# Kernel optimization log

Measured on AMD Instinct MI355X. Metric: run time of the kernel, lower is better.

The kernel has to match this reference:

```python
import jax, jax.numpy as jnp
import numpy as np

N, IN_DIM, H1, H2, HEADS = 3072, 256, 128, 64, 4
NEG_INF = -9.0e15  # matches torch zero_vec = -9e15

def _xavier(key, shape):
    fan_in, fan_out = shape[-2], shape[-1]
    lim = np.sqrt(6.0 / (fan_in + fan_out)).astype(np.float32)
    return jax.random.uniform(key, shape, jnp.float32, -lim, lim)

def setup_inputs() -> dict:
    key = jax.random.key(0)
    ks = jax.random.split(key, 14)
    x = jax.random.normal(ks[0], (N, IN_DIM), jnp.float32)
    adj = jax.random.randint(ks[1], (N, N), 0, 2, jnp.int32)
    # layer 1 params (per-head stacked)
    W1 = _xavier(ks[2], (HEADS, IN_DIM, H1))
    a1s = _xavier(ks[3], (HEADS, H1)) * 1.414   # a[:F] of the (2F,1) xavier vector
    a1d = _xavier(ks[4], (HEADS, H1)) * 1.414   # a[F:]
    lin1 = _xavier(ks[5], (HEADS * H1, H1))
    res1 = _xavier(ks[6], (IN_DIM, H1))
    # layer 2 params
    W2 = _xavier(ks[7], (HEADS, H1, H2))
    a2s = _xavier(ks[8], (HEADS, H2)) * 1.414
    a2d = _xavier(ks[9], (HEADS, H2)) * 1.414
    lin2 = _xavier(ks[10], (HEADS * H2, H2))
    res2 = _xavier(ks[11], (H1, H2))
    return {"x": x, "adj": adj, "W1": W1, "a1s": a1s, "a1d": a1d,
            "lin1": lin1, "res1": res1, "W2": W2, "a2s": a2s, "a2d": a2d,
            "lin2": lin2, "res2": res2}

def _gat_residual_layer(h, mask, W, a_s, a_d, lin, res):
    # h: [N, F_in], W: [H, F_in, F_out], mask: [N, N] bool
    Wh = jnp.einsum('nf,hfo->hno', h, W)                 # [H, N, F_out]
    src = jnp.einsum('hno,ho->hn', Wh, a_s)              # Wh @ a[:F]
    dst = jnp.einsum('hno,ho->hn', Wh, a_d)              # Wh @ a[F:]
    e = src[:, :, None] + dst[:, None, :]                # [H, N, N]
    e = jnp.where(e > 0, e, 0.2 * e)                     # leaky_relu(0.2)
    e = jnp.where(mask[None], e, NEG_INF)                # adj mask
    attn = jax.nn.softmax(e, axis=-1)                    # dropout p=0.1 -> identity (eval)
    hp = jax.nn.elu(jnp.einsum('hij,hjo->hio', attn, Wh))  # per-head output, elu
    n = h.shape[0]
    hp = jnp.transpose(hp, (1, 0, 2)).reshape(n, -1)     # concat heads (head-major)
    hp = jax.nn.elu(hp @ lin)                            # multi-head mix + elu
    out = jax.nn.relu(hp + h @ res)                      # residual + relu
    return jax.nn.relu(out)                              # encoder-loop relu; dropout(0.4) identity

def reference(x, adj, W1, a1s, a1d, lin1, res1, W2, a2s, a2d, lin2, res2):
    mask = adj > 0
    h = _gat_residual_layer(x, mask, W1, a1s, a1d, lin1, res1)
    h = _gat_residual_layer(h, mask, W2, a2s, a2d, lin2, res2)
    return h  # embedding [N, H2]
```

## Files before the change

kernel.cpp:

```cpp
#include <hip/hip_runtime.h>
#include <hip/hip_bf16.h>
#include <stdint.h>

using bf16 = __hip_bfloat16;
typedef short short8 __attribute__((ext_vector_type(8)));
typedef short short4v __attribute__((ext_vector_type(4)));
typedef float f32x4 __attribute__((ext_vector_type(4)));

constexpr int N = 3072;
constexpr int D0 = 256;
constexpr int F1 = 128;
constexpr int F2 = 64;
constexpr int HEADS = 4;
constexpr int NW = N / 32;
constexpr float CSHIFT = 20.0f;

#define DI __device__ __forceinline__
DI short f2bs(float v) { bf16 b = __float2bfloat16(v); return *(short*)&b; }

__global__ __launch_bounds__(256) void k_pack_adj(const int* __restrict__ adj,
                                                  uint32_t* __restrict__ bits) {
  int idx = blockIdx.x * 256 + threadIdx.x;
  unsigned long long m = __ballot(adj[idx] > 0);
  if ((threadIdx.x & 63) == 0) {
    bits[idx >> 5]       = (uint32_t)m;
    bits[(idx >> 5) + 1] = (uint32_t)(m >> 32);
  }
}

__global__ __launch_bounds__(256) void k_cvt(const float* __restrict__ x,
                                             const float* __restrict__ W1,
                                             const float* __restrict__ lin1,
                                             const float* __restrict__ res1,
                                             const float* __restrict__ W2,
                                             const float* __restrict__ lin2,
                                             const float* __restrict__ res2,
                                             bf16* __restrict__ xb,
                                             bf16* __restrict__ W1T,
                                             bf16* __restrict__ lin1T,
                                             bf16* __restrict__ res1T,
                                             bf16* __restrict__ W2T,
                                             bf16* __restrict__ lin2T,
                                             bf16* __restrict__ res2T) {
  int t = blockIdx.y;
  int i = blockIdx.x * 256 + threadIdx.x;
  switch (t) {
    case 0:
      if (i < N * D0) xb[i] = __float2bfloat16(x[i]);
      break;
    case 1:
      if (i < HEADS * F1 * D0) { int k = i & 255; int ho = i >> 8; int h = ho >> 7, o = ho & 127;
        W1T[i] = __float2bfloat16(W1[((size_t)h * D0 + k) * F1 + o]); }
      break;
    case 2:
      if (i < F1 * HEADS * F1) { int k = i & 511; int o = i >> 9;
        lin1T[i] = __float2bfloat16(lin1[k * F1 + o]); }
      break;
    case 3:
      if (i < F1 * D0) { int k = i & 255; int o = i >> 8;
        res1T[i] = __float2bfloat16(res1[k * F1 + o]); }
      break;
    case 4:
      if (i < HEADS * F2 * F1) { int k = i & 127; int ho = i >> 7; int h = ho >> 6, o = ho & 63;
        W2T[i] = __float2bfloat16(W2[((size_t)h * F1 + k) * F2 + o]); }
      break;
    case 5:
      if (i < F2 * HEADS * F2) { int k = i & 255; int o = i >> 8;
        lin2T[i] = __float2bfloat16(lin2[k * F2 + o]); }
      break;
    case 6:
      if (i < F2 * F1) { int k = i & 127; int o = i >> 7;
        res2T[i] = __float2bfloat16(res2[k * F2 + o]); }
      break;
  }
}

template <int K, int NOUT, int F>
__global__ __launch_bounds__(256) void k_whead_mfma(const bf16* __restrict__ A,
                                                    const bf16* __restrict__ BT,
                                                    bf16* __restrict__ BP,
                                                    const float* __restrict__ as_,
                                                    const float* __restrict__ ad_,
                                                    float* __restrict__ src,
                                                    float* __restrict__ dst) {
  int row0 = blockIdx.x * 16;
  int wid = threadIdx.x >> 6, lane = threadIdx.x & 63;
  int l15 = lane & 15, q = lane >> 4;
  int col = blockIdx.y * 64 + wid * 16 + l15;

  const bf16* aP = A + (size_t)(row0 + l15) * K + q * 8;
  const bf16* bP = BT + (size_t)col * K + q * 8;
  f32x4 acc;
#pragma unroll
  for (int r = 0; r < 4; r++) acc[r] = 0.f;
#pragma unroll
  for (int ks = 0; ks < K / 32; ks++) {
    short8 a = *(const short8*)(aP + ks * 32);
    short8 b = *(const short8*)(bP + ks * 32);
    acc = __builtin_amdgcn_mfma_f32_16x16x32_bf16(a, b, acc, 0, 0, 0);
  }

  int h  = col / F;
  int cl = col % F;
  int ct = cl >> 4;
  int jt = row0 >> 5;
  int qp = ((row0 >> 4) & 1) * 2 + (q >> 1);
  int eo = (q & 1) * 4;
  short4v w;
#pragma unroll
  for (int r = 0; r < 4; r++) w[r] = f2bs(acc[r]);
  size_t off = ((((size_t)h * (F / 16) + ct) * (N / 32) + jt) * 4 + qp) * 128 + l15 * 8 + eo;
  *(short4v*)(BP + off) = w;

  float asv = as_[col], adv = ad_[col];
#pragma unroll
  for (int r = 0; r < 4; r++) {
    float sp = acc[r] * asv, dp = acc[r] * adv;
#pragma unroll
    for (int m = 1; m < 16; m <<= 1) {
      sp += __shfl_xor(sp, m);
      dp += __shfl_xor(dp, m);
    }
    if (l15 == 0) {
      atomicAdd(&src[h * N + row0 + q * 4 + r], sp);
      atomicAdd(&dst[h * N + row0 + q * 4 + r], dp);
    }
  }
}

template <int F>
__global__ __launch_bounds__(256, 2) void k_attn_fused(const bf16* __restrict__ BP,
                                                       const float* __restrict__ src,
                                                       const float* __restrict__ dst,
                                                       const uint32_t* __restrict__ bits,
                                                       float* __restrict__ hp_part,
                                                       float* __restrict__ rs_part) {
  constexpr int CT = F / 16;
  constexpr int CTN = CT / 4;
  constexpr int KSTEPS = 12;
  int h    = blockIdx.y;
  int kb   = blockIdx.z;
  int row0 = blockIdx.x * 32;
  int tid = threadIdx.x, wid = tid >> 6, lane = tid & 63;
  int l15 = lane & 15, q = lane >> 4;
  int jbase = kb * (N / 2) + wid * 384;

  float src0 = src[h * N + row0 + l15];
  float src1 = src[h * N + row0 + 16 + l15];
  const float* dh = dst + h * N;
  const uint32_t* b0 = bits + (size_t)(row0 + l15) * NW;
  const uint32_t* b1 = bits + (size_t)(row0 + 16 + l15) * NW;
  const bf16* bph = BP + (size_t)h * CT * (N / 32) * 512;

  f32x4 acc0[CT], acc1[CT];
#pragma unroll
  for (int ct = 0; ct < CT; ct++)
#pragma unroll
    for (int r = 0; r < 4; r++) { acc0[ct][r] = 0.f; acc1[ct][r] = 0.f; }
  float rs0 = 0.f, rs1 = 0.f;

  for (int ks = 0; ks < KSTEPS; ks++) {
    int j0 = jbase + ks * 32;
    int jt = j0 >> 5;
    f32x4 dlo = *(const f32x4*)(dh + j0 + q * 8);
    f32x4 dhi = *(const f32x4*)(dh + j0 + q * 8 + 4);
    uint32_t m0 = (b0[jt] >> (q * 8)) & 0xffu;
    uint32_t m1 = (b1[jt] >> (q * 8)) & 0xffu;
    float pv0[8], pv1[8];
#pragma unroll
    for (int e = 0; e < 8; e++) {
      float d = e < 4 ? dlo[e] : dhi[e - 4];
      float t0 = src0 + d; t0 = fmaxf(t0, 0.2f * t0);
      float p0 = ((m0 >> e) & 1u) ? __expf(t0 - CSHIFT) : 0.f;
      rs0 += p0; pv0[e] = p0;
      float t1 = src1 + d; t1 = fmaxf(t1, 0.2f * t1);
      float p1 = ((m1 >> e) & 1u) ? __expf(t1 - CSHIFT) : 0.f;
      rs1 += p1; pv1[e] = p1;
    }
    short8 a0, a1;
#pragma unroll
    for (int e = 0; e < 8; e++) { a0[e] = f2bs(pv0[e]); a1[e] = f2bs(pv1[e]); }
#pragma unroll
    for (int ct = 0; ct < CT; ct++) {
      short8 b = *(const short8*)(bph + (((size_t)ct * (N / 32) + jt) * 64 + lane) * 8);
      acc0[ct] = __builtin_amdgcn_mfma_f32_16x16x32_bf16(a0, b, acc0[ct], 0, 0, 0);
      acc1[ct] = __builtin_amdgcn_mfma_f32_16x16x32_bf16(a1, b, acc1[ct], 0, 0, 0);
    }
  }

  rs0 += __shfl_xor(rs0, 16); rs0 += __shfl_xor(rs0, 32);
  rs1 += __shfl_xor(rs1, 16); rs1 += __shfl_xor(rs1, 32);
  if (q == 0) atomicAdd(&rs_part[((size_t)kb * HEADS + h) * N + row0 + l15], rs0);
  if (q == 1) atomicAdd(&rs_part[((size_t)kb * HEADS + h) * N + row0 + 16 + l15], rs1);

  __shared__ float red[4][64][CT * 4 + 1];
#pragma unroll
  for (int t = 0; t < 2; t++) {
    __syncthreads();
#pragma unroll
    for (int ct = 0; ct < CT; ct++)
#pragma unroll
      for (int r = 0; r < 4; r++)
        red[wid][lane][ct * 4 + r] = t ? acc1[ct][r] : acc0[ct][r];
    __syncthreads();
#pragma unroll
    for (int cc = 0; cc < CTN; cc++) {
      int ct = wid * CTN + cc;
#pragma unroll
      for (int r = 0; r < 4; r++) {
        float v = red[0][lane][ct * 4 + r] + red[1][lane][ct * 4 + r] +
                  red[2][lane][ct * 4 + r] + red[3][lane][ct * 4 + r];
        int row = row0 + t * 16 + q * 4 + r;
        hp_part[((size_t)kb * N + row) * (HEADS * F) + h * F + ct * 16 + l15] = v;
      }
    }
  }
}

template <int K1, int K2, int NOUT, int F, bool F32OUT>
__global__ __launch_bounds__(256) void k_mix_mfma(const float* __restrict__ hpp,
                                                  const float* __restrict__ rs,
                                                  const bf16* __restrict__ B1T,
                                                  const bf16* __restrict__ A2,
                                                  const bf16* __restrict__ B2T,
                                                  void* __restrict__ outv) {
  int row0 = blockIdx.x * 16;
  int wid = threadIdx.x >> 6, lane = threadIdx.x & 63;
  int l15 = lane & 15, q = lane >> 4;
  int col = blockIdx.y * 64 + wid * 16 + l15;
  int row = row0 + l15;

  f32x4 acc1, acc2;
#pragma unroll
  for (int r = 0; r < 4; r++) { acc1[r] = 0.f; acc2[r] = 0.f; }

  const float* p0 = hpp + (size_t)row * K1;
  const float* p1 = hpp + ((size_t)N + row) * K1;
  const bf16* b1P = B1T + (size_t)col * K1 + q * 8;
#pragma unroll
  for (int ks = 0; ks < K1 / 32; ks++) {
    int h = (ks * 32) / F;
    float s = rs[h * N + row] + rs[(HEADS + h) * N + row];
    float inv = 1.f / s;
    int c0k = ks * 32 + q * 8;
    f32x4 x0 = *(const f32x4*)(p0 + c0k);
    f32x4 x1 = *(const f32x4*)(p0 + c0k + 4);
    f32x4 y0 = *(const f32x4*)(p1 + c0k);
    f32x4 y1 = *(const f32x4*)(p1 + c0k + 4);
    short8 a;
#pragma unroll
    for (int e = 0; e < 4; e++) {
      float v = (x0[e] + y0[e]) * inv;
      v = v > 0.f ? v : __expf(v) - 1.f;
      a[e] = f2bs(v);
    }
#pragma unroll
    for (int e = 0; e < 4; e++) {
      float v = (x1[e] + y1[e]) * inv;
      v = v > 0.f ? v : __expf(v) - 1.f;
      a[4 + e] = f2bs(v);
    }
    short8 b = *(const short8*)(b1P + ks * 32);
    acc1 = __builtin_amdgcn_mfma_f32_16x16x32_bf16(a, b, acc1, 0, 0, 0);
  }

  const bf16* a2P = A2 + (size_t)row * K2 + q * 8;
  const bf16* b2P = B2T + (size_t)col * K2 + q * 8;
#pragma unroll
  for (int ks = 0; ks < K2 / 32; ks++) {
    short8 a = *(const short8*)(a2P + ks * 32);
    short8 b = *(const short8*)(b2P + ks * 32);
    acc2 = __builtin_amdgcn_mfma_f32_16x16x32_bf16(a, b, acc2, 0, 0, 0);
  }

#pragma unroll
  for (int r = 0; r < 4; r++) {
    float v = acc1[r];
    v = v > 0.f ? v : __expf(v) - 1.f;
    v += acc2[r];
    v = v > 0.f ? v : 0.f;
    int rw = row0 + q * 4 + r;
    if (F32OUT) ((float*)outv)[(size_t)rw * NOUT + col] = v;
    else        ((bf16*)outv)[(size_t)rw * NOUT + col] = __float2bfloat16(v);
  }
}

extern "C" void kernel_launch(void* const* d_in, const int* in_sizes, int n_in,
                              void* d_out, int out_size, void* d_ws, size_t ws_size,
                              hipStream_t stream) {
  const float* x    = (const float*)d_in[0];
  const int*   adj  = (const int*)d_in[1];
  const float* W1   = (const float*)d_in[2];
  const float* a1s  = (const float*)d_in[3];
  const float* a1d  = (const float*)d_in[4];
  const float* lin1 = (const float*)d_in[5];
  const float* res1 = (const float*)d_in[6];
  const float* W2   = (const float*)d_in[7];
  const float* a2s  = (const float*)d_in[8];
  const float* a2d  = (const float*)d_in[9];
  const float* lin2 = (const float*)d_in[10];
  const float* res2 = (const float*)d_in[11];
  float* out = (float*)d_out;

  char* p = (char*)d_ws;
  auto alloc = [&](size_t bytes) { void* r = (void*)p; p += (bytes + 255) & ~(size_t)255; return r; };
  uint32_t* bits = (uint32_t*)alloc((size_t)N * NW * 4);
  bf16* xb    = (bf16*)alloc((size_t)N * D0 * 2);
  bf16* W1T   = (bf16*)alloc((size_t)HEADS * F1 * D0 * 2);
  bf16* lin1T = (bf16*)alloc((size_t)F1 * HEADS * F1 * 2);
  bf16* res1T = (bf16*)alloc((size_t)F1 * D0 * 2);
  bf16* W2T   = (bf16*)alloc((size_t)HEADS * F2 * F1 * 2);
  bf16* lin2T = (bf16*)alloc((size_t)F2 * HEADS * F2 * 2);
  bf16* res2T = (bf16*)alloc((size_t)F2 * F1 * 2);
  bf16* BP1   = (bf16*)alloc((size_t)HEADS * F1 * N * 2);
  bf16* BP2   = (bf16*)alloc((size_t)HEADS * F2 * N * 2);
  float* src1 = (float*)alloc((size_t)HEADS * N * 4);
  float* dst1 = (float*)alloc((size_t)HEADS * N * 4);
  float* src2 = (float*)alloc((size_t)HEADS * N * 4);
  float* dst2 = (float*)alloc((size_t)HEADS * N * 4);
  float* rs1  = (float*)alloc((size_t)2 * HEADS * N * 4);
  float* rs2  = (float*)alloc((size_t)2 * HEADS * N * 4);
  float* hpp1 = (float*)alloc((size_t)2 * N * HEADS * F1 * 4);
  float* hpp2 = (float*)alloc((size_t)2 * N * HEADS * F2 * 4);
  bf16* h1b   = (bf16*)alloc((size_t)N * F1 * 2);

  hipMemsetAsync(src1, 0, (size_t)HEADS * N * 4 * 8, stream);

  k_pack_adj<<<dim3(N * N / 256), dim3(256), 0, stream>>>(adj, bits);
  k_cvt<<<dim3(N * D0 / 256, 7), dim3(256), 0, stream>>>(x, W1, lin1, res1, W2, lin2, res2,
                                                         xb, W1T, lin1T, res1T, W2T, lin2T, res2T);

  k_whead_mfma<D0, HEADS * F1, F1>
      <<<dim3(N / 16, HEADS * F1 / 64), dim3(256), 0, stream>>>(xb, W1T, BP1, a1s, a1d, src1, dst1);
  k_attn_fused<F1><<<dim3(N / 32, HEADS, 2), dim3(256), 0, stream>>>(BP1, src1, dst1, bits, hpp1, rs1);
  k_mix_mfma<HEADS * F1, D0, F1, F1, false>
      <<<dim3(N / 16, F1 / 64), dim3(256), 0, stream>>>(hpp1, rs1, lin1T, xb, res1T, h1b);

  k_whead_mfma<F1, HEADS * F2, F2>
      <<<dim3(N / 16, HEADS * F2 / 64), dim3(256), 0, stream>>>(h1b, W2T, BP2, a2s, a2d, src2, dst2);
  k_attn_fused<F2><<<dim3(N / 32, HEADS, 2), dim3(256), 0, stream>>>(BP2, src2, dst2, bits, hpp2, rs2);
  k_mix_mfma<HEADS * F2, F1, F2, F2, true>
      <<<dim3(N / 16, 1), dim3(256), 0, stream>>>(hpp2, rs2, lin2T, h1b, res2T, out);
}
```

Measured before the change: 215.2 us.

## Shrink attention row tile to 16 and use single-wave blocks for GEMMs

```diff
diff --git a/kernel.cpp b/kernel.cpp
--- a/kernel.cpp
+++ b/kernel.cpp
@@ -76,17 +76,17 @@
 }
 
 template <int K, int NOUT, int F>
-__global__ __launch_bounds__(256) void k_whead_mfma(const bf16* __restrict__ A,
-                                                    const bf16* __restrict__ BT,
-                                                    bf16* __restrict__ BP,
-                                                    const float* __restrict__ as_,
-                                                    const float* __restrict__ ad_,
-                                                    float* __restrict__ src,
-                                                    float* __restrict__ dst) {
+__global__ __launch_bounds__(64) void k_whead_mfma(const bf16* __restrict__ A,
+                                                   const bf16* __restrict__ BT,
+                                                   bf16* __restrict__ BP,
+                                                   const float* __restrict__ as_,
+                                                   const float* __restrict__ ad_,
+                                                   float* __restrict__ src,
+                                                   float* __restrict__ dst) {
   int row0 = blockIdx.x * 16;
-  int wid = threadIdx.x >> 6, lane = threadIdx.x & 63;
+  int lane = threadIdx.x;
   int l15 = lane & 15, q = lane >> 4;
-  int col = blockIdx.y * 64 + wid * 16 + l15;
+  int col = blockIdx.y * 16 + l15;
 
   const bf16* aP = A + (size_t)(row0 + l15) * K + q * 8;
   const bf16* bP = BT + (size_t)col * K + q * 8;
@@ -129,35 +129,33 @@
 }
 
 template <int F>
-__global__ __launch_bounds__(256, 2) void k_attn_fused(const bf16* __restrict__ BP,
-                                                       const float* __restrict__ src,
-                                                       const float* __restrict__ dst,
-                                                       const uint32_t* __restrict__ bits,
-                                                       float* __restrict__ hp_part,
-                                                       float* __restrict__ rs_part) {
+__global__ __launch_bounds__(256) void k_attn_fused(const bf16* __restrict__ BP,
+                                                    const float* __restrict__ src,
+                                                    const float* __restrict__ dst,
+                                                    const uint32_t* __restrict__ bits,
+                                                    float* __restrict__ hp_part,
+                                                    float* __restrict__ rs_part) {
   constexpr int CT = F / 16;
   constexpr int CTN = CT / 4;
   constexpr int KSTEPS = 12;
   int h    = blockIdx.y;
   int kb   = blockIdx.z;
-  int row0 = blockIdx.x * 32;
+  int row0 = blockIdx.x * 16;
   int tid = threadIdx.x, wid = tid >> 6, lane = tid & 63;
   int l15 = lane & 15, q = lane >> 4;
   int jbase = kb * (N / 2) + wid * 384;
 
   float src0 = src[h * N + row0 + l15];
-  float src1 = src[h * N + row0 + 16 + l15];
   const float* dh = dst + h * N;
   const uint32_t* b0 = bits + (size_t)(row0 + l15) * NW;
-  const uint32_t* b1 = bits + (size_t)(row0 + 16 + l15) * NW;
   const bf16* bph = BP + (size_t)h * CT * (N / 32) * 512;
 
-  f32x4 acc0[CT], acc1[CT];
+  f32x4 acc0[CT];
 #pragma unroll
   for (int ct = 0; ct < CT; ct++)
 #pragma unroll
-    for (int r = 0; r < 4; r++) { acc0[ct][r] = 0.f; acc1[ct][r] = 0.f; }
-  float rs0 = 0.f, rs1 = 0.f;
+    for (int r = 0; r < 4; r++) acc0[ct][r] = 0.f;
+  float rs0 = 0.f;
 
   for (int ks = 0; ks < KSTEPS; ks++) {
     int j0 = jbase + ks * 32;
@@ -165,69 +163,57 @@
     f32x4 dlo = *(const f32x4*)(dh + j0 + q * 8);
     f32x4 dhi = *(const f32x4*)(dh + j0 + q * 8 + 4);
     uint32_t m0 = (b0[jt] >> (q * 8)) & 0xffu;
-    uint32_t m1 = (b1[jt] >> (q * 8)) & 0xffu;
-    float pv0[8], pv1[8];
+    float pv0[8];
 #pragma unroll
     for (int e = 0; e < 8; e++) {
       float d = e < 4 ? dlo[e] : dhi[e - 4];
       float t0 = src0 + d; t0 = fmaxf(t0, 0.2f * t0);
       float p0 = ((m0 >> e) & 1u) ? __expf(t0 - CSHIFT) : 0.f;
       rs0 += p0; pv0[e] = p0;
-      float t1 = src1 + d; t1 = fmaxf(t1, 0.2f * t1);
-      float p1 = ((m1 >> e) & 1u) ? __expf(t1 - CSHIFT) : 0.f;
-      rs1 += p1; pv1[e] = p1;
-    }
-    short8 a0, a1;
-#pragma unroll
-    for (int e = 0; e < 8; e++) { a0[e] = f2bs(pv0[e]); a1[e] = f2bs(pv1[e]); }
+    }
+    short8 a0;
+#pragma unroll
+    for (int e = 0; e < 8; e++) a0[e] = f2bs(pv0[e]);
 #pragma unroll
     for (int ct = 0; ct < CT; ct++) {
       short8 b = *(const short8*)(bph + (((size_t)ct * (N / 32) + jt) * 64 + lane) * 8);
       acc0[ct] = __builtin_amdgcn_mfma_f32_16x16x32_bf16(a0, b, acc0[ct], 0, 0, 0);
-      acc1[ct] = __builtin_amdgcn_mfma_f32_16x16x32_bf16(a1, b, acc1[ct], 0, 0, 0);
     }
   }
 
   rs0 += __shfl_xor(rs0, 16); rs0 += __shfl_xor(rs0, 32);
-  rs1 += __shfl_xor(rs1, 16); rs1 += __shfl_xor(rs1, 32);
   if (q == 0) atomicAdd(&rs_part[((size_t)kb * HEADS + h) * N + row0 + l15], rs0);
-  if (q == 1) atomicAdd(&rs_part[((size_t)kb * HEADS + h) * N + row0 + 16 + l15], rs1);
 
   __shared__ float red[4][64][CT * 4 + 1];
 #pragma unroll
-  for (int t = 0; t < 2; t++) {
-    __syncthreads();
-#pragma unroll
-    for (int ct = 0; ct < CT; ct++)
-#pragma unroll
-      for (int r = 0; r < 4; r++)
-        red[wid][lane][ct * 4 + r] = t ? acc1[ct][r] : acc0[ct][r];
-    __syncthreads();
-#pragma unroll
-    for (int cc = 0; cc < CTN; cc++) {
-      int ct = wid * CTN + cc;
-#pragma unroll
-      for (int r = 0; r < 4; r++) {
-        float v = red[0][lane][ct * 4 + r] + red[1][lane][ct * 4 + r] +
-                  red[2][lane][ct * 4 + r] + red[3][lane][ct * 4 + r];
-        int row = row0 + t * 16 + q * 4 + r;
-        hp_part[((size_t)kb * N + row) * (HEADS * F) + h * F + ct * 16 + l15] = v;
-      }
+  for (int ct = 0; ct < CT; ct++)
+#pragma unroll
+    for (int r = 0; r < 4; r++) red[wid][lane][ct * 4 + r] = acc0[ct][r];
+  __syncthreads();
+#pragma unroll
+  for (int cc = 0; cc < CTN; cc++) {
+    int ct = wid * CTN + cc;
+#pragma unroll
+    for (int r = 0; r < 4; r++) {
+      float v = red[0][lane][ct * 4 + r] + red[1][lane][ct * 4 + r] +
+                red[2][lane][ct * 4 + r] + red[3][lane][ct * 4 + r];
+      int row = row0 + q * 4 + r;
+      hp_part[((size_t)kb * N + row) * (HEADS * F) + h * F + ct * 16 + l15] = v;
     }
   }
 }
 
 template <int K1, int K2, int NOUT, int F, bool F32OUT>
-__global__ __launch_bounds__(256) void k_mix_mfma(const float* __restrict__ hpp,
-                                                  const float* __restrict__ rs,
-                                                  const bf16* __restrict__ B1T,
-                                                  const bf16* __restrict__ A2,
-                                                  const bf16* __restrict__ B2T,
-                                                  void* __restrict__ outv) {
+__global__ __launch_bounds__(64) void k_mix_mfma(const float* __restrict__ hpp,
+                                                 const float* __restrict__ rs,
+                                                 const bf16* __restrict__ B1T,
+                                                 const bf16* __restrict__ A2,
+                                                 const bf16* __restrict__ B2T,
+                                                 void* __restrict__ outv) {
   int row0 = blockIdx.x * 16;
-  int wid = threadIdx.x >> 6, lane = threadIdx.x & 63;
+  int lane = threadIdx.x;
   int l15 = lane & 15, q = lane >> 4;
-  int col = blockIdx.y * 64 + wid * 16 + l15;
+  int col = blockIdx.y * 16 + l15;
   int row = row0 + l15;
 
   f32x4 acc1, acc2;
@@ -331,14 +317,14 @@
                                                          xb, W1T, lin1T, res1T, W2T, lin2T, res2T);
 
   k_whead_mfma<D0, HEADS * F1, F1>
-      <<<dim3(N / 16, HEADS * F1 / 64), dim3(256), 0, stream>>>(xb, W1T, BP1, a1s, a1d, src1, dst1);
-  k_attn_fused<F1><<<dim3(N / 32, HEADS, 2), dim3(256), 0, stream>>>(BP1, src1, dst1, bits, hpp1, rs1);
+      <<<dim3(N / 16, HEADS * F1 / 16), dim3(64), 0, stream>>>(xb, W1T, BP1, a1s, a1d, src1, dst1);
+  k_attn_fused<F1><<<dim3(N / 16, HEADS, 2), dim3(256), 0, stream>>>(BP1, src1, dst1, bits, hpp1, rs1);
   k_mix_mfma<HEADS * F1, D0, F1, F1, false>
-      <<<dim3(N / 16, F1 / 64), dim3(256), 0, stream>>>(hpp1, rs1, lin1T, xb, res1T, h1b);
+      <<<dim3(N / 16, F1 / 16), dim3(64), 0, stream>>>(hpp1, rs1, lin1T, xb, res1T, h1b);
 
   k_whead_mfma<F1, HEADS * F2, F2>
-      <<<dim3(N / 16, HEADS * F2 / 64), dim3(256), 0, stream>>>(h1b, W2T, BP2, a2s, a2d, src2, dst2);
-  k_attn_fused<F2><<<dim3(N / 32, HEADS, 2), dim3(256), 0, stream>>>(BP2, src2, dst2, bits, hpp2, rs2);
+      <<<dim3(N / 16, HEADS * F2 / 16), dim3(64), 0, stream>>>(h1b, W2T, BP2, a2s, a2d, src2, dst2);
+  k_attn_fused<F2><<<dim3(N / 16, HEADS, 2), dim3(256), 0, stream>>>(BP2, src2, dst2, bits, hpp2, rs2);
   k_mix_mfma<HEADS * F2, F1, F2, F2, true>
-      <<<dim3(N / 16, 1), dim3(256), 0, stream>>>(hpp2, rs2, lin2T, h1b, res2T, out);
-}
+      <<<dim3(N / 16, F2 / 16), dim3(64), 0, stream>>>(hpp2, rs2, lin2T, h1b, res2T, out);
+}
```

Measured after the change: 221.6 us. 3.0% more time.
